# Kernel tuning notes

Measured on AMD Instinct MI355X. Metric: run time of the kernel, lower is better.

The kernel has to match this reference:

```python
import jax, jax.numpy as jnp
import numpy as np
import math

D_MODEL = 512
NUM_HEADS = 8
MAX_LEN = 10000.0


def positional_encoding_2d(seq_len, d_model, H, W, dtype=jnp.float32):
    # position along height repeated across width, and vice versa
    pos_h = jnp.repeat(jnp.arange(H, dtype=dtype), W)  # [H*W]
    pos_w = jnp.tile(jnp.arange(W, dtype=dtype), H)    # [H*W]
    div_term = jnp.exp(jnp.arange(0, d_model, 2, dtype=dtype) * (-(math.log(MAX_LEN) / d_model)))
    div = div_term[: d_model // 4]  # [d_model//4]
    pe = jnp.zeros((seq_len, d_model), dtype=dtype)
    pe = pe.at[:, 0::4].set(jnp.sin(pos_h[:, None] * div))
    pe = pe.at[:, 1::4].set(jnp.cos(pos_h[:, None] * div))
    pe = pe.at[:, 2::4].set(jnp.sin(pos_w[:, None] * div))
    pe = pe.at[:, 3::4].set(jnp.cos(pos_w[:, None] * div))
    return pe


def setup_inputs() -> dict:
    key = jax.random.key(0)
    ks = jax.random.split(key, 6)
    B, C, H, W = 8, D_MODEL, 32, 32
    d = D_MODEL
    s = 1.0 / math.sqrt(d)
    x = jax.random.normal(ks[0], (B, C, H, W), dtype=jnp.float32)
    Wq = jax.random.normal(ks[1], (d, d), dtype=jnp.float32) * s
    Wk = jax.random.normal(ks[2], (d, d), dtype=jnp.float32) * s
    Wv = jax.random.normal(ks[3], (d, d), dtype=jnp.float32) * s
    Wo = jax.random.normal(ks[4], (d, d), dtype=jnp.float32) * s
    bo = jnp.zeros((d,), dtype=jnp.float32)
    gamma = jnp.ones((d,), dtype=jnp.float32)
    beta = jnp.zeros((d,), dtype=jnp.float32)
    return {"x": x, "Wq": Wq, "Wk": Wk, "Wv": Wv, "Wo": Wo, "bo": bo, "gamma": gamma, "beta": beta}


def reference(x, Wq, Wk, Wv, Wo, bo, gamma, beta):
    B, C, H, W = x.shape
    d_model = C
    nh = NUM_HEADS
    dk = d_model // nh
    seq = H * W

    # [B, C, H, W] -> [B, seq, d_model]
    x_seq = x.reshape(B, C, seq).transpose(0, 2, 1)
    pe = positional_encoding_2d(seq, d_model, H, W, dtype=x.dtype)
    x_seq = x_seq + pe[None]
    residual = x_seq

    # QKV projections (torch Linear: y = x @ W.T)
    q = (x_seq @ Wq.T).reshape(B, seq, nh, dk).transpose(0, 2, 1, 3)  # [B, nh, S, dk]
    k = (x_seq @ Wk.T).reshape(B, seq, nh, dk).transpose(0, 2, 1, 3)
    v = (x_seq @ Wv.T).reshape(B, seq, nh, dk).transpose(0, 2, 1, 3)

    scores = jnp.einsum("bhsd,bhtd->bhst", q, k) / math.sqrt(dk)  # [B, nh, S, S]
    weights = jax.nn.softmax(scores, axis=-1)
    # dropout is identity at inference
    attn = jnp.einsum("bhst,bhtd->bhsd", weights, v)  # [B, nh, S, dk]
    attn = attn.transpose(0, 2, 1, 3).reshape(B, seq, d_model)

    out = attn @ Wo.T + bo
    y = out + residual
    mean = jnp.mean(y, axis=-1, keepdims=True)
    var = jnp.var(y, axis=-1, keepdims=True)
    y = (y - mean) / jnp.sqrt(var + 1e-5) * gamma + beta

    return y.transpose(0, 2, 1).reshape(B, C, H, W)
```

## Files before the change

kernel.cpp:

```cpp
#include <hip/hip_runtime.h>
#include <hip/hip_bf16.h>
#include <math.h>

#define DEV static __device__ __forceinline__

typedef unsigned short u16;
typedef unsigned int u32;
typedef __attribute__((ext_vector_type(4))) float f32x4;
typedef __attribute__((ext_vector_type(16))) float f32x16;
typedef __attribute__((ext_vector_type(8))) __bf16 bf16x8;
typedef __attribute__((ext_vector_type(4))) u16 u16x4;
typedef __attribute__((ext_vector_type(4))) u32 u32x4;

DEV u16 f2bf(float f) {
  unsigned u = __float_as_uint(f);
  u += 0x7fffu + ((u >> 16) & 1u);
  return (u16)(u >> 16);
}
DEV float bf2f(u16 x) { return __uint_as_float((u32)x << 16); }

DEV float fexp2(float x) { return __builtin_amdgcn_exp2f(x); }

DEV u32 cvt_pk_bf16(float lo, float hi) {
  u32 r;
  asm("v_cvt_pk_bf16_f32 %0, %1, %2" : "=v"(r) : "v"(lo), "v"(hi));
  return r;
}

DEV void perm32swap(u32& a, u32& b) {
  asm("v_permlane32_swap_b32 %0, %1" : "+v"(a), "+v"(b));
}

DEV void gl2lds16(const void* g, void* l) {
  __builtin_amdgcn_global_load_lds(
      (const __attribute__((address_space(1))) void*)g,
      (__attribute__((address_space(3))) void*)l, 16, 0, 0);
}

template<int RPW>
DEV void stage_rows(const u16* __restrict__ g, int gstride, u16* lds, int wave, int lane) {
  const int r_in = lane >> 3, slot = lane & 7;
  const int base_row = wave * RPW;
#pragma unroll
  for (int i = 0; i < RPW / 8; ++i) {
    const int row = base_row + i * 8 + r_in;
    const int sslot = slot ^ (row & 7);
    gl2lds16(g + (size_t)row * gstride + sslot * 8,
             lds + (size_t)(base_row + i * 8) * 64);
  }
}

DEV bf16x8 frag_read(const u16* lds, int row, int kslot) {
  const int slot = kslot ^ (row & 7);
  return *(const bf16x8*)(lds + row * 64 + slot * 8);
}

DEV f32x4 mfma16(bf16x8 a, bf16x8 b, f32x4 c) {
  return __builtin_amdgcn_mfma_f32_16x16x32_bf16(a, b, c, 0, 0, 0);
}
DEV f32x16 mfma32(bf16x8 a, bf16x8 b, f32x16 c) {
  return __builtin_amdgcn_mfma_f32_32x32x16_bf16(a, b, c, 0, 0, 0);
}

__global__ __launch_bounds__(256) void convert_w(
    const float* __restrict__ w0, const float* __restrict__ w1,
    const float* __restrict__ w2, const float* __restrict__ w3,
    u16* __restrict__ dst) {
  const float* src = (blockIdx.y == 0) ? w0 : (blockIdx.y == 1) ? w1
                   : (blockIdx.y == 2) ? w2 : w3;
  const size_t base = (size_t)blockIdx.y * 262144;
  const int i = (blockIdx.x * 256 + threadIdx.x) * 4;
  f32x4 v = *(const f32x4*)(src + i);
  u16x4 o;
  o.x = f2bf(v.x); o.y = f2bf(v.y); o.z = f2bf(v.z); o.w = f2bf(v.w);
  *(u16x4*)(dst + base + i) = o;
}

__global__ __launch_bounds__(256) void prep_x(
    const float* __restrict__ x, u16* __restrict__ Xp) {
  __shared__ float tile[32][33];
  const int b = blockIdx.z, c0 = blockIdx.y * 32, s0 = blockIdx.x * 32;
  const int t = threadIdx.x;
  const int cf = t >> 5, sf = t & 31;
#pragma unroll
  for (int i = 0; i < 4; ++i) {
    const int c = c0 + cf + i * 8;
    tile[cf + i * 8][sf] = x[((size_t)b * 512 + c) * 1024 + s0 + sf];
  }
  __syncthreads();
  const int cl = t & 31, sl = t >> 5;
  const int cg = c0 + cl;
  const int j = cg >> 2;
  const float dv = expf((float)j * (-9.210340371976184f / 256.0f));
#pragma unroll
  for (int i = 0; i < 4; ++i) {
    const int s = s0 + sl + i * 8;
    const float pos = (cg & 2) ? (float)(s & 31) : (float)(s >> 5);
    const float arg = pos * dv;
    const float pe = (cg & 1) ? cosf(arg) : sinf(arg);
    const float v = tile[cl][sl + i * 8] + pe;
    Xp[((size_t)b * 1024 + s) * 512 + cg] = f2bf(v);
  }
}

__global__ __launch_bounds__(256) void gemm_qkv(
    const u16* __restrict__ Xp, const u16* __restrict__ Wb,
    u16* __restrict__ Qb, u16* __restrict__ Kb, u16* __restrict__ Vtb,
    float qscale) {
  __shared__ __align__(16) u16 smem[128 * 132];
  u16* As = smem;
  u16* Bs = smem + 128 * 64;
  const int t = threadIdx.x, lane = t & 63, wave = t >> 6;
  const int bn0 = blockIdx.x * 128, bm0 = blockIdx.y * 128;
  const int wr = wave >> 1, wc = wave & 1;
  const u16* Ag = Xp + (size_t)bm0 * 512;
  const u16* Bg = Wb + (size_t)bn0 * 512;
  f32x4 acc[4][4] = {};
  for (int kt = 0; kt < 512; kt += 64) {
    __syncthreads();
    stage_rows<32>(Ag + kt, 512, As, wave, lane);
    stage_rows<32>(Bg + kt, 512, Bs, wave, lane);
    __syncthreads();
#pragma unroll
    for (int ks = 0; ks < 2; ++ks) {
      bf16x8 af[4], bfr[4];
#pragma unroll
      for (int m = 0; m < 4; ++m)
        af[m] = frag_read(As, wr * 64 + m * 16 + (lane & 15), ks * 4 + (lane >> 4));
#pragma unroll
      for (int n = 0; n < 4; ++n)
        bfr[n] = frag_read(Bs, wc * 64 + n * 16 + (lane & 15), ks * 4 + (lane >> 4));
#pragma unroll
      for (int m = 0; m < 4; ++m)
#pragma unroll
        for (int n = 0; n < 4; ++n)
          acc[m][n] = mfma16(af[m], bfr[n], acc[m][n]);
    }
  }
  const int cl = lane & 15, rg = (lane >> 4) * 4;
  if (bn0 >= 1024) {
    __syncthreads();
#pragma unroll
    for (int m = 0; m < 4; ++m)
#pragma unroll
      for (int n = 0; n < 4; ++n) {
        const int dvL = wc * 64 + n * 16 + cl;
        const int rowL0 = wr * 64 + m * 16 + rg;
        u16x4 pk;
#pragma unroll
        for (int r = 0; r < 4; ++r) pk[r] = f2bf(acc[m][n][r]);
        *(u16x4*)(smem + dvL * 132 + rowL0) = pk;
      }
    __syncthreads();
    const int dvg0 = bn0 - 1024;
#pragma unroll
    for (int i = 0; i < 16; ++i) {
      const int idx = i * 256 + t;
      const int dv = idx >> 5, ch = (idx & 31) * 4;
      const u16x4 v = *(const u16x4*)(smem + dv * 132 + ch);
      *(u16x4*)(Vtb + (size_t)(dvg0 + dv) * 8192 + bm0 + ch) = v;
    }
  } else {
    u16* dst = (bn0 >= 512) ? Kb : Qb;
    const float al = (bn0 >= 512) ? 1.0f : qscale;
    const int cb = (bn0 & 511) + wc * 64;
#pragma unroll
    for (int m = 0; m < 4; ++m)
#pragma unroll
      for (int n = 0; n < 4; ++n) {
        const int col = cb + n * 16 + cl;
#pragma unroll
        for (int r = 0; r < 4; ++r) {
          const int row = bm0 + wr * 64 + m * 16 + rg + r;
          dst[(size_t)row * 512 + col] = f2bf(acc[m][n][r] * al);
        }
      }
  }
}

__global__ __launch_bounds__(256) void gemm_out(
    const u16* __restrict__ A, const u16* __restrict__ Bt,
    u16* __restrict__ ypre16, const float* __restrict__ bias,
    const u16* __restrict__ residb) {
  __shared__ __align__(16) u16 As[128 * 64];
  __shared__ __align__(16) u16 Bs[64 * 64];
  const int t = threadIdx.x, lane = t & 63, wave = t >> 6;
  const int bn0 = blockIdx.x * 64, bm0 = blockIdx.y * 128;
  const int wr = wave >> 1, wc = wave & 1;
  const u16* Ag = A + (size_t)bm0 * 512;
  const u16* Bg = Bt + (size_t)bn0 * 512;
  f32x4 acc[4][2] = {};
  for (int kt = 0; kt < 512; kt += 64) {
    __syncthreads();
    stage_rows<32>(Ag + kt, 512, As, wave, lane);
    stage_rows<16>(Bg + kt, 512, Bs, wave, lane);
    __syncthreads();
#pragma unroll
    for (int ks = 0; ks < 2; ++ks) {
      bf16x8 af[4], bfr[2];
#pragma unroll
      for (int m = 0; m < 4; ++m)
        af[m] = frag_read(As, wr * 64 + m * 16 + (lane & 15), ks * 4 + (lane >> 4));
#pragma unroll
      for (int n = 0; n < 2; ++n)
        bfr[n] = frag_read(Bs, wc * 32 + n * 16 + (lane & 15), ks * 4 + (lane >> 4));
#pragma unroll
      for (int m = 0; m < 4; ++m)
#pragma unroll
        for (int n = 0; n < 2; ++n)
          acc[m][n] = mfma16(af[m], bfr[n], acc[m][n]);
    }
  }
  const int cl = lane & 15, rg = (lane >> 4) * 4;
#pragma unroll
  for (int m = 0; m < 4; ++m)
#pragma unroll
    for (int n = 0; n < 2; ++n) {
      const int col = bn0 + wc * 32 + n * 16 + cl;
#pragma unroll
      for (int r = 0; r < 4; ++r) {
        const int row = bm0 + wr * 64 + m * 16 + rg + r;
        const float v = acc[m][n][r] + bias[col] + bf2f(residb[(size_t)row * 512 + col]);
        ypre16[(size_t)row * 512 + col] = f2bf(v);
      }
    }
}

__global__ __launch_bounds__(256, 4) void attn(
    const u16* __restrict__ Qb, const u16* __restrict__ Kb,
    const u16* __restrict__ Vt, u16* __restrict__ Ob) {
  __shared__ __align__(16) u16 Ks[2][64 * 64];
  __shared__ __align__(16) u16 Vs[2][64 * 64];
  const int t = threadIdx.x, lane = t & 63, wave = t >> 6;
  const int wg = blockIdx.x;
  const int b = wg & 7, h = (wg >> 3) & 7, qt = wg >> 6;
  const int qsub = wave & 1, half = wave >> 1;
  const int ql = lane & 31, hl = lane >> 5;
  const int q0 = qt * 64 + qsub * 32;
  bf16x8 bq[4];
  {
    const u16* qrow = Qb + ((size_t)b * 1024 + q0 + ql) * 512 + h * 64 + hl * 8;
#pragma unroll
    for (int c = 0; c < 4; ++c) bq[c] = *(const bf16x8*)(qrow + c * 16);
  }
  f32x16 ot[2] = {};
  float m_run = -1e30f, l_run = 0.f;
  u16* stg_dst = qsub ? Vs[half] : Ks[half];
  for (int i = 0; i < 8; ++i) {
    const int kb = half * 512 + i * 64;
    {
      const int r_in = lane >> 3, slot = lane & 7;
      const u16* src; size_t gs;
      if (qsub) { src = Vt + (size_t)(h * 64) * 8192 + (size_t)b * 1024 + kb; gs = 8192; }
      else      { src = Kb + ((size_t)b * 1024 + kb) * 512 + h * 64;          gs = 512; }
#pragma unroll
      for (int j = 0; j < 8; ++j) {
        const int row = j * 8 + r_in;
        const int ss = slot ^ (row & 7);
        gl2lds16(src + (size_t)row * gs + ss * 8, stg_dst + j * 512);
      }
    }
    __syncthreads();
    f32x16 st[2] = {};
    __builtin_amdgcn_s_setprio(1);
#pragma unroll
    for (int c = 0; c < 4; ++c) {
      bf16x8 a0 = frag_read(Ks[half], ql, c * 2 + hl);
      bf16x8 a1 = frag_read(Ks[half], 32 + ql, c * 2 + hl);
      st[0] = mfma32(a0, bq[c], st[0]);
      st[1] = mfma32(a1, bq[c], st[1]);
    }
    __builtin_amdgcn_s_setprio(0);
    float m0[8];
#pragma unroll
    for (int i2 = 0; i2 < 8; ++i2)
      m0[i2] = fmaxf(fmaxf(st[0][i2], st[0][i2 + 8]), fmaxf(st[1][i2], st[1][i2 + 8]));
#pragma unroll
    for (int i2 = 0; i2 < 4; ++i2) m0[i2] = fmaxf(m0[i2], m0[i2 + 4]);
    float mx = fmaxf(fmaxf(m0[0], m0[1]), fmaxf(m0[2], m0[3]));
    mx = fmaxf(mx, __shfl_xor(mx, 32));
    if (!__all(mx <= m_run + 8.f)) {
      const float mn = fmaxf(m_run, mx);
      const float sc = fexp2(m_run - mn);
      m_run = mn;
      l_run *= sc;
      ot[0] *= sc;
      ot[1] *= sc;
    }
#pragma unroll
    for (int i2 = 0; i2 < 16; ++i2) {
      st[0][i2] = fexp2(st[0][i2] - m_run);
      st[1][i2] = fexp2(st[1][i2] - m_run);
    }
    float s0[8];
#pragma unroll
    for (int i2 = 0; i2 < 8; ++i2)
      s0[i2] = (st[0][i2] + st[0][i2 + 8]) + (st[1][i2] + st[1][i2 + 8]);
#pragma unroll
    for (int i2 = 0; i2 < 4; ++i2) s0[i2] = s0[i2] + s0[i2 + 4];
    float rs = (s0[0] + s0[1]) + (s0[2] + s0[3]);
    rs += __shfl_xor(rs, 32);
    l_run += rs;
    __builtin_amdgcn_s_setprio(1);
#pragma unroll
    for (int c = 0; c < 4; ++c) {
      const int kf = c >> 1, i0 = (c & 1) * 4;
      u32 w0 = cvt_pk_bf16(st[kf][2 * i0 + 0], st[kf][2 * i0 + 1]);
      u32 w1 = cvt_pk_bf16(st[kf][2 * i0 + 2], st[kf][2 * i0 + 3]);
      u32 w2 = cvt_pk_bf16(st[kf][2 * i0 + 4], st[kf][2 * i0 + 5]);
      u32 w3 = cvt_pk_bf16(st[kf][2 * i0 + 6], st[kf][2 * i0 + 7]);
      perm32swap(w0, w2);
      perm32swap(w1, w3);
      u32x4 wv; wv.x = w0; wv.y = w1; wv.z = w2; wv.w = w3;
      bf16x8 bp = *(bf16x8*)&wv;
      bf16x8 v0 = frag_read(Vs[half], ql, c * 2 + hl);
      bf16x8 v1 = frag_read(Vs[half], 32 + ql, c * 2 + hl);
      ot[0] = mfma32(v0, bp, ot[0]);
      ot[1] = mfma32(v1, bp, ot[1]);
    }
    __builtin_amdgcn_s_setprio(0);
    __syncthreads();
  }
  float* Om = (float*)&Ks[0][0] + qsub * 2048;
  float* Ml = (float*)&Vs[0][0];
  if (wave >= 2) {
#pragma unroll
    for (int df = 0; df < 2; ++df)
#pragma unroll
      for (int r = 0; r < 16; ++r) {
        const int dr = (r & 3) + 8 * (r >> 2) + 4 * hl;
        Om[(df * 32 + dr) * 32 + ql] = ot[df][r];
      }
    if (hl == 0) {
      Ml[qsub * 64 + ql] = m_run;
      Ml[qsub * 64 + 32 + ql] = l_run;
    }
    __syncthreads();
  } else {
    __syncthreads();
    const float m2 = Ml[qsub * 64 + ql];
    const float l2 = Ml[qsub * 64 + 32 + ql];
    const float m = fmaxf(m_run, m2);
    const float a = fexp2(m_run - m);
    const float bsc = fexp2(m2 - m);
    const float inv = 1.f / (l_run * a + l2 * bsc);
    u16* orow = Ob + ((size_t)b * 1024 + q0 + ql) * 512 + h * 64;
#pragma unroll
    for (int df = 0; df < 2; ++df)
#pragma unroll
      for (int r = 0; r < 16; ++r) {
        const int dr = (r & 3) + 8 * (r >> 2) + 4 * hl;
        const float v = ot[df][r] * a + Om[(df * 32 + dr) * 32 + ql] * bsc;
        orow[df * 32 + dr] = f2bf(v * inv);
      }
  }
}

__global__ __launch_bounds__(256) void ln_out(
    const u16* __restrict__ ypre16, const float* __restrict__ gamma,
    const float* __restrict__ beta, float* __restrict__ out) {
  __shared__ float tile[16 * 513];
  __shared__ float stats[16][2];
  const int b = blockIdx.y, s0 = blockIdx.x * 16;
  const int t = threadIdx.x, lane = t & 63, wave = t >> 6;
  const u16* src = ypre16 + ((size_t)b * 1024 + s0) * 512;
#pragma unroll
  for (int i = 0; i < 8; ++i) {
    const int idx = i * 256 + t;
    const int flat = idx * 4;
    const int row = flat >> 9, col = flat & 511;
    const u16x4 v = *(const u16x4*)(src + flat);
    float* d = tile + row * 513 + col;
    d[0] = bf2f(v.x); d[1] = bf2f(v.y); d[2] = bf2f(v.z); d[3] = bf2f(v.w);
  }
  __syncthreads();
#pragma unroll
  for (int i = 0; i < 4; ++i) {
    const int r = wave * 4 + i;
    float sum = 0.f, sq = 0.f;
#pragma unroll
    for (int k = 0; k < 8; ++k) {
      const float v = tile[r * 513 + lane + 64 * k];
      sum += v; sq += v * v;
    }
#pragma unroll
    for (int off = 32; off >= 1; off >>= 1) {
      sum += __shfl_xor(sum, off);
      sq  += __shfl_xor(sq, off);
    }
    if (lane == 0) {
      const float mean = sum * (1.f / 512.f);
      const float var = sq * (1.f / 512.f) - mean * mean;
      stats[r][0] = mean;
      stats[r][1] = rsqrtf(var + 1e-5f);
    }
  }
  __syncthreads();
  const int sl = t & 15, cg = t >> 4;
  float* outb = out + (size_t)b * 512 * 1024 + s0;
  const float mean = stats[sl][0], rstd = stats[sl][1];
#pragma unroll 4
  for (int i = 0; i < 32; ++i) {
    const int c = i * 16 + cg;
    const float v = (tile[sl * 513 + c] - mean) * rstd;
    outb[(size_t)c * 1024 + sl] = v * gamma[c] + beta[c];
  }
}

extern "C" void kernel_launch(void* const* d_in, const int* in_sizes, int n_in,
                              void* d_out, int out_size, void* d_ws, size_t ws_size,
                              hipStream_t stream) {
  const float* x     = (const float*)d_in[0];
  const float* Wq    = (const float*)d_in[1];
  const float* Wk    = (const float*)d_in[2];
  const float* Wv    = (const float*)d_in[3];
  const float* Wo    = (const float*)d_in[4];
  const float* bo    = (const float*)d_in[5];
  const float* gamma = (const float*)d_in[6];
  const float* beta  = (const float*)d_in[7];
  char* ws = (char*)d_ws;
  const size_t MB = 1048576;
  u16*   Xp    = (u16*)(ws);
  u16*   Wb    = (u16*)(ws + 8 * MB);
  u16*   Qb    = (u16*)(ws + 10 * MB);
  u16*   Kb    = (u16*)(ws + 18 * MB);
  u16*   Vtb   = (u16*)(ws + 26 * MB);
  u16*   Ob    = (u16*)(ws + 34 * MB);
  u16*   ypre  = (u16*)(ws + 42 * MB);

  convert_w<<<dim3(256, 4), 256, 0, stream>>>(Wq, Wk, Wv, Wo, Wb);
  prep_x<<<dim3(32, 16, 8), 256, 0, stream>>>(x, Xp);
  gemm_qkv<<<dim3(12, 64), 256, 0, stream>>>(Xp, Wb, Qb, Kb, Vtb,
                                             0.125f * 1.44269504088896f);
  attn<<<1024, 256, 0, stream>>>(Qb, Kb, Vtb, Ob);
  gemm_out<<<dim3(8, 64), 256, 0, stream>>>(Ob, Wb + 3 * 262144, ypre, bo, Xp);
  ln_out<<<dim3(64, 8), 256, 0, stream>>>(ypre, gamma, beta, (float*)d_out);
}
```

Measured before the change: 95.38 us.

## Store K/V in MFMA fragment layout and load attention operands directly to registers

The QKV GEMM epilogue now writes K and V in a pre-swizzled per-(batch, head, key-tile) MFMA fragment order, so each lane can load its operand with one contiguous 16-byte read. The attention kernel drops LDS staging and block barriers. Each wave handles 32 queries over the full key range and double-buffers K fragments in registers, with 128 queries per block and half as many blocks. This also removes the cross-wave split-K merge through shared memory. In exchange it uses more registers (launch bounds lowered to 2), K/V reads are repeated per wave instead of shared through LDS, and there is less parallelism per query tile.

```diff
diff --git a/kernel.cpp b/kernel.cpp
--- a/kernel.cpp
+++ b/kernel.cpp
@@ -105,7 +105,7 @@
 
 __global__ __launch_bounds__(256) void gemm_qkv(
     const u16* __restrict__ Xp, const u16* __restrict__ Wb,
-    u16* __restrict__ Qb, u16* __restrict__ Kb, u16* __restrict__ Vtb,
+    u16* __restrict__ Qb, u16* __restrict__ Kf, u16* __restrict__ Vf,
     float qscale) {
   __shared__ __align__(16) u16 smem[128 * 132];
   u16* As = smem;
@@ -138,43 +138,71 @@
     }
   }
   const int cl = lane & 15, rg = (lane >> 4) * 4;
-  if (bn0 >= 1024) {
-    __syncthreads();
+  if (bn0 < 512) {
 #pragma unroll
     for (int m = 0; m < 4; ++m)
 #pragma unroll
       for (int n = 0; n < 4; ++n) {
-        const int dvL = wc * 64 + n * 16 + cl;
-        const int rowL0 = wr * 64 + m * 16 + rg;
-        u16x4 pk;
-#pragma unroll
-        for (int r = 0; r < 4; ++r) pk[r] = f2bf(acc[m][n][r]);
-        *(u16x4*)(smem + dvL * 132 + rowL0) = pk;
-      }
-    __syncthreads();
-    const int dvg0 = bn0 - 1024;
-#pragma unroll
-    for (int i = 0; i < 16; ++i) {
-      const int idx = i * 256 + t;
-      const int dv = idx >> 5, ch = (idx & 31) * 4;
-      const u16x4 v = *(const u16x4*)(smem + dv * 132 + ch);
-      *(u16x4*)(Vtb + (size_t)(dvg0 + dv) * 8192 + bm0 + ch) = v;
-    }
-  } else {
-    u16* dst = (bn0 >= 512) ? Kb : Qb;
-    const float al = (bn0 >= 512) ? 1.0f : qscale;
-    const int cb = (bn0 & 511) + wc * 64;
-#pragma unroll
-    for (int m = 0; m < 4; ++m)
-#pragma unroll
-      for (int n = 0; n < 4; ++n) {
-        const int col = cb + n * 16 + cl;
+        const int col = bn0 + wc * 64 + n * 16 + cl;
 #pragma unroll
         for (int r = 0; r < 4; ++r) {
           const int row = bm0 + wr * 64 + m * 16 + rg + r;
-          dst[(size_t)row * 512 + col] = f2bf(acc[m][n][r] * al);
+          Qb[(size_t)row * 512 + col] = f2bf(acc[m][n][r] * qscale);
         }
       }
+  } else {
+    const bool isK = (bn0 < 1024);
+    __syncthreads();
+    if (isK) {
+#pragma unroll
+      for (int m = 0; m < 4; ++m)
+#pragma unroll
+        for (int n = 0; n < 4; ++n) {
+          const int col = wc * 64 + n * 16 + cl;
+#pragma unroll
+          for (int r = 0; r < 4; ++r) {
+            const int row = wr * 64 + m * 16 + rg + r;
+            smem[row * 132 + col] = f2bf(acc[m][n][r]);
+          }
+        }
+    } else {
+#pragma unroll
+      for (int m = 0; m < 4; ++m)
+#pragma unroll
+        for (int n = 0; n < 4; ++n) {
+          const int dvL = wc * 64 + n * 16 + cl;
+          const int rowL0 = wr * 64 + m * 16 + rg;
+          u16x4 pk;
+#pragma unroll
+          for (int r = 0; r < 4; ++r) pk[r] = f2bf(acc[m][n][r]);
+          *(u16x4*)(smem + dvL * 132 + rowL0) = pk;
+        }
+    }
+    __syncthreads();
+    const int b = bm0 >> 10;
+    const int s0 = bm0 & 1023;
+    const int hbase = isK ? ((bn0 - 512) >> 6) : ((bn0 - 1024) >> 6);
+    u16* dstb = isK ? Kf : Vf;
+    const int ql = lane & 31, hl = lane >> 5;
+#pragma unroll
+    for (int pass = 0; pass < 8; ++pass) {
+      const int fidx = pass * 4 + wave;
+      const int rh = fidx & 1;
+      const int c = (fidx >> 1) & 3;
+      const int head_local = (fidx >> 3) & 1;
+      const int kt_local = (fidx >> 4) & 1;
+      int row_l, col_l;
+      if (isK) { row_l = kt_local * 64 + rh * 32 + ql; col_l = head_local * 64 + c * 16 + hl * 8; }
+      else     { row_l = head_local * 64 + rh * 32 + ql; col_l = kt_local * 64 + c * 16 + hl * 8; }
+      const u16x4 lo = *(const u16x4*)(smem + row_l * 132 + col_l);
+      const u16x4 hi = *(const u16x4*)(smem + row_l * 132 + col_l + 4);
+      const int h = hbase + head_local;
+      const int ktg = (s0 >> 6) + kt_local;
+      const size_t fi = (size_t)(((b * 8 + h) * 16 + ktg) * 8 + c * 2 + rh);
+      u16* dst = dstb + fi * 512 + lane * 8;
+      *(u16x4*)(dst) = lo;
+      *(u16x4*)(dst + 4) = hi;
+    }
   }
 }
 
@@ -226,51 +254,43 @@
     }
 }
 
-__global__ __launch_bounds__(256, 4) void attn(
-    const u16* __restrict__ Qb, const u16* __restrict__ Kb,
-    const u16* __restrict__ Vt, u16* __restrict__ Ob) {
-  __shared__ __align__(16) u16 Ks[2][64 * 64];
-  __shared__ __align__(16) u16 Vs[2][64 * 64];
+__global__ __launch_bounds__(256, 2) void attn(
+    const u16* __restrict__ Qb, const u16* __restrict__ Kf,
+    const u16* __restrict__ Vf, u16* __restrict__ Ob) {
   const int t = threadIdx.x, lane = t & 63, wave = t >> 6;
   const int wg = blockIdx.x;
   const int b = wg & 7, h = (wg >> 3) & 7, qt = wg >> 6;
-  const int qsub = wave & 1, half = wave >> 1;
   const int ql = lane & 31, hl = lane >> 5;
-  const int q0 = qt * 64 + qsub * 32;
+  const int q0 = qt * 128 + wave * 32;
   bf16x8 bq[4];
   {
     const u16* qrow = Qb + ((size_t)b * 1024 + q0 + ql) * 512 + h * 64 + hl * 8;
 #pragma unroll
     for (int c = 0; c < 4; ++c) bq[c] = *(const bf16x8*)(qrow + c * 16);
   }
+  const u16* fb = Kf + (size_t)((b * 8 + h) * 16) * 8 * 512;
+  const u16* vb = Vf + (size_t)((b * 8 + h) * 16) * 8 * 512;
   f32x16 ot[2] = {};
   float m_run = -1e30f, l_run = 0.f;
-  u16* stg_dst = qsub ? Vs[half] : Ks[half];
-  for (int i = 0; i < 8; ++i) {
-    const int kb = half * 512 + i * 64;
-    {
-      const int r_in = lane >> 3, slot = lane & 7;
-      const u16* src; size_t gs;
-      if (qsub) { src = Vt + (size_t)(h * 64) * 8192 + (size_t)b * 1024 + kb; gs = 8192; }
-      else      { src = Kb + ((size_t)b * 1024 + kb) * 512 + h * 64;          gs = 512; }
-#pragma unroll
-      for (int j = 0; j < 8; ++j) {
-        const int row = j * 8 + r_in;
-        const int ss = slot ^ (row & 7);
-        gl2lds16(src + (size_t)row * gs + ss * 8, stg_dst + j * 512);
-      }
-    }
-    __syncthreads();
+  bf16x8 ka[8], kb_[8], va[8];
+#pragma unroll
+  for (int f = 0; f < 8; ++f)
+    ka[f] = *(const bf16x8*)(fb + (size_t)f * 512 + lane * 8);
+
+  auto tile_step = [&](int tt, bf16x8* kc, bf16x8* kn) {
+#pragma unroll
+    for (int f = 0; f < 8; ++f)
+      va[f] = *(const bf16x8*)(vb + ((size_t)(tt * 8 + f)) * 512 + lane * 8);
+    const int tn = (tt + 1) & 15;
+#pragma unroll
+    for (int f = 0; f < 8; ++f)
+      kn[f] = *(const bf16x8*)(fb + ((size_t)(tn * 8 + f)) * 512 + lane * 8);
     f32x16 st[2] = {};
-    __builtin_amdgcn_s_setprio(1);
 #pragma unroll
     for (int c = 0; c < 4; ++c) {
-      bf16x8 a0 = frag_read(Ks[half], ql, c * 2 + hl);
-      bf16x8 a1 = frag_read(Ks[half], 32 + ql, c * 2 + hl);
-      st[0] = mfma32(a0, bq[c], st[0]);
-      st[1] = mfma32(a1, bq[c], st[1]);
-    }
-    __builtin_amdgcn_s_setprio(0);
+      st[0] = mfma32(kc[2 * c], bq[c], st[0]);
+      st[1] = mfma32(kc[2 * c + 1], bq[c], st[1]);
+    }
     float m0[8];
 #pragma unroll
     for (int i2 = 0; i2 < 8; ++i2)
@@ -282,10 +302,8 @@
     if (!__all(mx <= m_run + 8.f)) {
       const float mn = fmaxf(m_run, mx);
       const float sc = fexp2(m_run - mn);
-      m_run = mn;
-      l_run *= sc;
-      ot[0] *= sc;
-      ot[1] *= sc;
+      m_run = mn; l_run *= sc;
+      ot[0] *= sc; ot[1] *= sc;
     }
 #pragma unroll
     for (int i2 = 0; i2 < 16; ++i2) {
@@ -301,7 +319,6 @@
     float rs = (s0[0] + s0[1]) + (s0[2] + s0[3]);
     rs += __shfl_xor(rs, 32);
     l_run += rs;
-    __builtin_amdgcn_s_setprio(1);
 #pragma unroll
     for (int c = 0; c < 4; ++c) {
       const int kf = c >> 1, i0 = (c & 1) * 4;
@@ -313,47 +330,25 @@
       perm32swap(w1, w3);
       u32x4 wv; wv.x = w0; wv.y = w1; wv.z = w2; wv.w = w3;
       bf16x8 bp = *(bf16x8*)&wv;
-      bf16x8 v0 = frag_read(Vs[half], ql, c * 2 + hl);
-      bf16x8 v1 = frag_read(Vs[half], 32 + ql, c * 2 + hl);
-      ot[0] = mfma32(v0, bp, ot[0]);
-      ot[1] = mfma32(v1, bp, ot[1]);
-    }
-    __builtin_amdgcn_s_setprio(0);
-    __syncthreads();
-  }
-  float* Om = (float*)&Ks[0][0] + qsub * 2048;
-  float* Ml = (float*)&Vs[0][0];
-  if (wave >= 2) {
-#pragma unroll
-    for (int df = 0; df < 2; ++df)
-#pragma unroll
-      for (int r = 0; r < 16; ++r) {
-        const int dr = (r & 3) + 8 * (r >> 2) + 4 * hl;
-        Om[(df * 32 + dr) * 32 + ql] = ot[df][r];
-      }
-    if (hl == 0) {
-      Ml[qsub * 64 + ql] = m_run;
-      Ml[qsub * 64 + 32 + ql] = l_run;
-    }
-    __syncthreads();
-  } else {
-    __syncthreads();
-    const float m2 = Ml[qsub * 64 + ql];
-    const float l2 = Ml[qsub * 64 + 32 + ql];
-    const float m = fmaxf(m_run, m2);
-    const float a = fexp2(m_run - m);
-    const float bsc = fexp2(m2 - m);
-    const float inv = 1.f / (l_run * a + l2 * bsc);
-    u16* orow = Ob + ((size_t)b * 1024 + q0 + ql) * 512 + h * 64;
-#pragma unroll
-    for (int df = 0; df < 2; ++df)
-#pragma unroll
-      for (int r = 0; r < 16; ++r) {
-        const int dr = (r & 3) + 8 * (r >> 2) + 4 * hl;
-        const float v = ot[df][r] * a + Om[(df * 32 + dr) * 32 + ql] * bsc;
-        orow[df * 32 + dr] = f2bf(v * inv);
-      }
-  }
+      ot[0] = mfma32(va[2 * c], bp, ot[0]);
+      ot[1] = mfma32(va[2 * c + 1], bp, ot[1]);
+    }
+  };
+  for (int tp = 0; tp < 8; ++tp) {
+    tile_step(2 * tp, ka, kb_);
+    tile_step(2 * tp + 1, kb_, ka);
+  }
+  const float inv = 1.f / l_run;
+  u16* orow = Ob + ((size_t)b * 1024 + q0 + ql) * 512 + h * 64;
+#pragma unroll
+  for (int df = 0; df < 2; ++df)
+#pragma unroll
+    for (int rq = 0; rq < 4; ++rq) {
+      u16x4 pk;
+#pragma unroll
+      for (int j = 0; j < 4; ++j) pk[j] = f2bf(ot[df][rq * 4 + j] * inv);
+      *(u16x4*)(orow + df * 32 + rq * 8 + 4 * hl) = pk;
+    }
 }
 
 __global__ __launch_bounds__(256) void ln_out(
@@ -423,16 +418,16 @@
   u16*   Xp    = (u16*)(ws);
   u16*   Wb    = (u16*)(ws + 8 * MB);
   u16*   Qb    = (u16*)(ws + 10 * MB);
-  u16*   Kb    = (u16*)(ws + 18 * MB);
-  u16*   Vtb   = (u16*)(ws + 26 * MB);
+  u16*   Kfr   = (u16*)(ws + 18 * MB);
+  u16*   Vfr   = (u16*)(ws + 26 * MB);
   u16*   Ob    = (u16*)(ws + 34 * MB);
   u16*   ypre  = (u16*)(ws + 42 * MB);
 
   convert_w<<<dim3(256, 4), 256, 0, stream>>>(Wq, Wk, Wv, Wo, Wb);
   prep_x<<<dim3(32, 16, 8), 256, 0, stream>>>(x, Xp);
-  gemm_qkv<<<dim3(12, 64), 256, 0, stream>>>(Xp, Wb, Qb, Kb, Vtb,
+  gemm_qkv<<<dim3(12, 64), 256, 0, stream>>>(Xp, Wb, Qb, Kfr, Vfr,
                                              0.125f * 1.44269504088896f);
-  attn<<<1024, 256, 0, stream>>>(Qb, Kb, Vtb, Ob);
+  attn<<<512, 256, 0, stream>>>(Qb, Kfr, Vfr, Ob);
   gemm_out<<<dim3(8, 64), 256, 0, stream>>>(Ob, Wb + 3 * 262144, ypre, bo, Xp);
   ln_out<<<dim3(64, 8), 256, 0, stream>>>(ypre, gamma, beta, (float*)d_out);
 }
```

After: 100.8 us. 5.7% more time.

## Fuse output projection GEMM with residual add and LayerNorm

Applied to the files above, without the earlier changes.

Replaces the separate gemm_out and ln_out kernels with one kernel in which each block computes a full 32-row by 512-column output tile. It adds bias and residual, reduces row statistics across waves, and writes the normalized, transposed result directly. This removes the bf16 intermediate buffer round trip and one kernel launch. In exchange the grid shrinks to 256 blocks with large shared memory, so B-tile staging per block grows and occupancy may drop.

```diff
diff --git a/kernel.cpp b/kernel.cpp
--- a/kernel.cpp
+++ b/kernel.cpp
@@ -178,52 +178,103 @@
   }
 }
 
-__global__ __launch_bounds__(256) void gemm_out(
+__global__ __launch_bounds__(256) void gemm_ln(
     const u16* __restrict__ A, const u16* __restrict__ Bt,
-    u16* __restrict__ ypre16, const float* __restrict__ bias,
-    const u16* __restrict__ residb) {
-  __shared__ __align__(16) u16 As[128 * 64];
-  __shared__ __align__(16) u16 Bs[64 * 64];
+    const u16* __restrict__ residb, const float* __restrict__ bias,
+    const float* __restrict__ gamma, const float* __restrict__ beta,
+    float* __restrict__ out) {
+  __shared__ __align__(16) u16 smem[34816];
+  __shared__ float redsum[4][32], redsq[4][32], srow[32][2];
   const int t = threadIdx.x, lane = t & 63, wave = t >> 6;
-  const int bn0 = blockIdx.x * 64, bm0 = blockIdx.y * 128;
-  const int wr = wave >> 1, wc = wave & 1;
-  const u16* Ag = A + (size_t)bm0 * 512;
-  const u16* Bg = Bt + (size_t)bn0 * 512;
-  f32x4 acc[4][2] = {};
+  const int m0 = blockIdx.x * 32;
+  const int b = m0 >> 10, s0 = m0 & 1023;
+  u16* As = smem;
+  u16* Bs = smem + 2048;
+  const u16* Ag = A + (size_t)m0 * 512;
+  f32x4 acc[2][8] = {};
   for (int kt = 0; kt < 512; kt += 64) {
     __syncthreads();
-    stage_rows<32>(Ag + kt, 512, As, wave, lane);
-    stage_rows<16>(Bg + kt, 512, Bs, wave, lane);
+    stage_rows<8>(Ag + kt, 512, As, wave, lane);
+    stage_rows<128>(Bt + kt, 512, Bs, wave, lane);
     __syncthreads();
 #pragma unroll
     for (int ks = 0; ks < 2; ++ks) {
-      bf16x8 af[4], bfr[2];
-#pragma unroll
-      for (int m = 0; m < 4; ++m)
-        af[m] = frag_read(As, wr * 64 + m * 16 + (lane & 15), ks * 4 + (lane >> 4));
-#pragma unroll
-      for (int n = 0; n < 2; ++n)
-        bfr[n] = frag_read(Bs, wc * 32 + n * 16 + (lane & 15), ks * 4 + (lane >> 4));
-#pragma unroll
-      for (int m = 0; m < 4; ++m)
-#pragma unroll
-        for (int n = 0; n < 2; ++n)
+      bf16x8 af[2], bfr[8];
+#pragma unroll
+      for (int m = 0; m < 2; ++m)
+        af[m] = frag_read(As, m * 16 + (lane & 15), ks * 4 + (lane >> 4));
+#pragma unroll
+      for (int n = 0; n < 8; ++n)
+        bfr[n] = frag_read(Bs, wave * 128 + n * 16 + (lane & 15), ks * 4 + (lane >> 4));
+#pragma unroll
+      for (int m = 0; m < 2; ++m)
+#pragma unroll
+        for (int n = 0; n < 8; ++n)
           acc[m][n] = mfma16(af[m], bfr[n], acc[m][n]);
     }
   }
+  __syncthreads();
+  float* fsm = (float*)smem;
+  float* fw = fsm + wave * (128 * 33);
   const int cl = lane & 15, rg = (lane >> 4) * 4;
-#pragma unroll
-  for (int m = 0; m < 4; ++m)
-#pragma unroll
-    for (int n = 0; n < 2; ++n) {
-      const int col = bn0 + wc * 32 + n * 16 + cl;
+  float psum[8], psq[8];
+#pragma unroll
+  for (int i = 0; i < 8; ++i) { psum[i] = 0.f; psq[i] = 0.f; }
+#pragma unroll
+  for (int m = 0; m < 2; ++m)
+#pragma unroll
+    for (int n = 0; n < 8; ++n) {
+      const int col_l = n * 16 + cl;
+      const int col = wave * 128 + col_l;
+      const float bi = bias[col];
 #pragma unroll
       for (int r = 0; r < 4; ++r) {
-        const int row = bm0 + wr * 64 + m * 16 + rg + r;
-        const float v = acc[m][n][r] + bias[col] + bf2f(residb[(size_t)row * 512 + col]);
-        ypre16[(size_t)row * 512 + col] = f2bf(v);
-      }
-    }
+        const int row_l = m * 16 + rg + r;
+        const float v = acc[m][n][r] + bi
+                      + bf2f(residb[(size_t)(m0 + row_l) * 512 + col]);
+        fw[col_l * 33 + row_l] = v;
+        psum[m * 4 + r] += v;
+        psq[m * 4 + r] += v * v;
+      }
+    }
+#pragma unroll
+  for (int i = 0; i < 8; ++i) {
+#pragma unroll
+    for (int off = 8; off >= 1; off >>= 1) {
+      psum[i] += __shfl_xor(psum[i], off);
+      psq[i]  += __shfl_xor(psq[i], off);
+    }
+  }
+  if (cl == 0) {
+#pragma unroll
+    for (int m = 0; m < 2; ++m)
+#pragma unroll
+      for (int r = 0; r < 4; ++r) {
+        const int row_l = m * 16 + rg + r;
+        redsum[wave][row_l] = psum[m * 4 + r];
+        redsq[wave][row_l]  = psq[m * 4 + r];
+      }
+  }
+  __syncthreads();
+  if (t < 32) {
+    float s = redsum[0][t] + redsum[1][t] + redsum[2][t] + redsum[3][t];
+    float q = redsq[0][t] + redsq[1][t] + redsq[2][t] + redsq[3][t];
+    const float mean = s * (1.f / 512.f);
+    const float var = q * (1.f / 512.f) - mean * mean;
+    srow[t][0] = mean;
+    srow[t][1] = rsqrtf(var + 1e-5f);
+  }
+  __syncthreads();
+  const int row = lane & 31, chalf = lane >> 5;
+  const float mean = srow[row][0], rstd = srow[row][1];
+  float* outb = out + (size_t)b * 512 * 1024 + s0 + row;
+#pragma unroll 4
+  for (int cc = 0; cc < 64; ++cc) {
+    const int col_l = cc * 2 + chalf;
+    const int col = wave * 128 + col_l;
+    const float v = (fw[col_l * 33 + row] - mean) * rstd;
+    outb[(size_t)col * 1024] = v * gamma[col] + beta[col];
+  }
 }
 
 __global__ __launch_bounds__(256, 4) void attn(
@@ -353,57 +404,6 @@
         const float v = ot[df][r] * a + Om[(df * 32 + dr) * 32 + ql] * bsc;
         orow[df * 32 + dr] = f2bf(v * inv);
       }
-  }
-}
-
-__global__ __launch_bounds__(256) void ln_out(
-    const u16* __restrict__ ypre16, const float* __restrict__ gamma,
-    const float* __restrict__ beta, float* __restrict__ out) {
-  __shared__ float tile[16 * 513];
-  __shared__ float stats[16][2];
-  const int b = blockIdx.y, s0 = blockIdx.x * 16;
-  const int t = threadIdx.x, lane = t & 63, wave = t >> 6;
-  const u16* src = ypre16 + ((size_t)b * 1024 + s0) * 512;
-#pragma unroll
-  for (int i = 0; i < 8; ++i) {
-    const int idx = i * 256 + t;
-    const int flat = idx * 4;
-    const int row = flat >> 9, col = flat & 511;
-    const u16x4 v = *(const u16x4*)(src + flat);
-    float* d = tile + row * 513 + col;
-    d[0] = bf2f(v.x); d[1] = bf2f(v.y); d[2] = bf2f(v.z); d[3] = bf2f(v.w);
-  }
-  __syncthreads();
-#pragma unroll
-  for (int i = 0; i < 4; ++i) {
-    const int r = wave * 4 + i;
-    float sum = 0.f, sq = 0.f;
-#pragma unroll
-    for (int k = 0; k < 8; ++k) {
-      const float v = tile[r * 513 + lane + 64 * k];
-      sum += v; sq += v * v;
-    }
-#pragma unroll
-    for (int off = 32; off >= 1; off >>= 1) {
-      sum += __shfl_xor(sum, off);
-      sq  += __shfl_xor(sq, off);
-    }
-    if (lane == 0) {
-      const float mean = sum * (1.f / 512.f);
-      const float var = sq * (1.f / 512.f) - mean * mean;
-      stats[r][0] = mean;
-      stats[r][1] = rsqrtf(var + 1e-5f);
-    }
-  }
-  __syncthreads();
-  const int sl = t & 15, cg = t >> 4;
-  float* outb = out + (size_t)b * 512 * 1024 + s0;
-  const float mean = stats[sl][0], rstd = stats[sl][1];
-#pragma unroll 4
-  for (int i = 0; i < 32; ++i) {
-    const int c = i * 16 + cg;
-    const float v = (tile[sl * 513 + c] - mean) * rstd;
-    outb[(size_t)c * 1024 + sl] = v * gamma[c] + beta[c];
   }
 }
 
@@ -426,13 +426,12 @@
   u16*   Kb    = (u16*)(ws + 18 * MB);
   u16*   Vtb   = (u16*)(ws + 26 * MB);
   u16*   Ob    = (u16*)(ws + 34 * MB);
-  u16*   ypre  = (u16*)(ws + 42 * MB);
 
   convert_w<<<dim3(256, 4), 256, 0, stream>>>(Wq, Wk, Wv, Wo, Wb);
   prep_x<<<dim3(32, 16, 8), 256, 0, stream>>>(x, Xp);
   gemm_qkv<<<dim3(12, 64), 256, 0, stream>>>(Xp, Wb, Qb, Kb, Vtb,
                                              0.125f * 1.44269504088896f);
   attn<<<1024, 256, 0, stream>>>(Qb, Kb, Vtb, Ob);
-  gemm_out<<<dim3(8, 64), 256, 0, stream>>>(Ob, Wb + 3 * 262144, ypre, bo, Xp);
-  ln_out<<<dim3(64, 8), 256, 0, stream>>>(ypre, gamma, beta, (float*)d_out);
-}
+  gemm_ln<<<256, 256, 0, stream>>>(Ob, Wb + 3 * 262144, Xp, bo, gamma, beta,
+                                   (float*)d_out);
+}
```

New measurement: 94.16 us. No clear change (-1.3%).
